# Optimization experiments

Hardware: AMD Instinct MI355X
Metric: run time of the kernel (lower is better)

The kernel has to match this reference:

```python
import jax, jax.numpy as jnp
import numpy as np

N = 100000       # num nodes
E = 1600000      # num edges (avg degree 16)
IN, HID, OUT, C = 128, 64, 64, 16


def setup_inputs() -> dict:
    key = jax.random.key(0)
    ks = jax.random.split(key, 10)
    x = jax.random.normal(ks[0], (N, IN), jnp.float32)
    edge_index = jax.random.randint(ks[1], (2, E), 0, N, dtype=jnp.int32)
    dict_node = jax.random.randint(ks[2], (N,), 0, N, dtype=jnp.int32)
    # learned parameters (Glorot-ish scaling)
    W1 = jax.random.normal(ks[3], (IN, HID), jnp.float32) / np.sqrt(IN)
    b1 = jnp.zeros((HID,), jnp.float32)
    W2 = jax.random.normal(ks[4], (HID, OUT), jnp.float32) / np.sqrt(HID)
    b2 = jnp.zeros((OUT,), jnp.float32)
    Wfc = jax.random.normal(ks[5], (OUT, C), jnp.float32) / np.sqrt(OUT)
    bfc = jnp.zeros((C,), jnp.float32)
    return {"x": x, "edge_index": edge_index, "dict_node": dict_node,
            "W1": W1, "b1": b1, "W2": W2, "b2": b2, "Wfc": Wfc, "bfc": bfc}


def _gcn_conv(h_in, W, b, src, dst, n):
    """GCNConv: D^-1/2 (A+I) D^-1/2 (X W) + b, self-loops handled analytically."""
    h = h_in @ W                                   # [N, F]
    deg = jax.ops.segment_sum(jnp.ones((src.shape[0],), h.dtype), dst,
                              num_segments=n) + 1.0  # +1 self-loop
    dinv = jax.lax.rsqrt(deg)                      # [N]
    norm = dinv[src] * dinv[dst]                   # [E]
    agg = jax.ops.segment_sum(h[src] * norm[:, None], dst, num_segments=n)
    agg = agg + h * (dinv * dinv)[:, None]         # self-loop contribution
    return agg + b


def reference(x, edge_index, dict_node, W1, b1, W2, b2, Wfc, bfc):
    n = x.shape[0]
    src, dst = edge_index[0], edge_index[1]
    h = jax.nn.relu(_gcn_conv(x, W1, b1, src, dst, n))
    # dropout p=0.5 is identity at inference
    h = jax.nn.relu(_gcn_conv(h, W2, b2, src, dst, n))
    # global_mean_pool over dict_node with size = num_nodes
    cnt = jax.ops.segment_sum(jnp.ones((n,), h.dtype), dict_node, num_segments=n)
    summ = jax.ops.segment_sum(h, dict_node, num_segments=n)
    pooled = summ / jnp.maximum(cnt, 1.0)[:, None]
    logits = pooled @ Wfc + bfc
    return jax.nn.log_softmax(logits, axis=1)
```

## Files before the change

kernel.cpp:

```cpp
#include <hip/hip_runtime.h>

#define THREADS 256
#define B1 256

typedef __attribute__((ext_vector_type(8))) short bf16x8;
typedef __attribute__((ext_vector_type(4))) float f32x4;
typedef __attribute__((ext_vector_type(2))) unsigned int u32x2;

__device__ inline ushort f2bf(float v) {
    union { float f; unsigned u; } a; a.f = v;
    unsigned r = a.u + 0x7fff + ((a.u >> 16) & 1);
    return (ushort)(r >> 16);
}
__device__ inline unsigned pack2(float a, float b) {
    return (unsigned)f2bf(a) | ((unsigned)f2bf(b) << 16);
}


__global__ void k_p1(const int* __restrict__ dst, int* __restrict__ pc,
                     int E, int NB, int chunk) {
    __shared__ int hist[512];
    int tid = threadIdx.x, blk = blockIdx.x;
    for (int i = tid; i < NB; i += THREADS) hist[i] = 0;
    __syncthreads();
    int e0 = blk * chunk;
    int e1 = e0 + chunk; if (e1 > E) e1 = E;
    for (int e = e0 + tid; e < e1; e += THREADS)
        atomicAdd(&hist[dst[e] >> 8], 1);
    __syncthreads();
    for (int i = tid; i < NB; i += THREADS) pc[i * B1 + blk] = hist[i];
}

__global__ void k_s1(int* __restrict__ pc, int* __restrict__ bsums, int total) {
    __shared__ int s[1024];
    int t = threadIdx.x;
    int idx = blockIdx.x * 1024 + t;
    int v = (idx < total) ? pc[idx] : 0;
    s[t] = v;
    __syncthreads();
    for (int o = 1; o < 1024; o <<= 1) {
        int x = (t >= (unsigned)o) ? s[t - o] : 0;
        __syncthreads();
        s[t] += x;
        __syncthreads();
    }
    if (idx < total) pc[idx] = s[t] - v;
    if (t == 1023) bsums[blockIdx.x] = s[1023];
}

__global__ void k_s2(int* __restrict__ bsums, int nb) {
    __shared__ int s[128];
    int t = threadIdx.x;
    int v = (t < nb) ? bsums[t] : 0;
    s[t] = v;
    __syncthreads();
    for (int o = 1; o < 128; o <<= 1) {
        int x = (t >= (unsigned)o) ? s[t - o] : 0;
        __syncthreads();
        s[t] += x;
        __syncthreads();
    }
    if (t < nb) bsums[t] = s[t] - v;
}

__global__ void k_p2(const int* __restrict__ src, const int* __restrict__ dst,
                     const int* __restrict__ pc, const int* __restrict__ bsx,
                     unsigned long long* __restrict__ part, int E, int NB, int chunk) {
    __shared__ int cur[512];
    int tid = threadIdx.x, blk = blockIdx.x;
    for (int i = tid; i < NB; i += THREADS) {
        int idx = i * B1 + blk;
        cur[i] = pc[idx] + bsx[idx >> 10];
    }
    __syncthreads();
    int e0 = blk * chunk;
    int e1 = e0 + chunk; if (e1 > E) e1 = E;
    for (int e = e0 + tid; e < e1; e += THREADS) {
        int d = dst[e], sv = src[e];
        int pos = atomicAdd(&cur[d >> 8], 1);
        part[pos] = ((unsigned long long)(unsigned)d << 32) | (unsigned)sv;
    }
}

__global__ void k_p3(const unsigned long long* __restrict__ part,
                     const int* __restrict__ pc, const int* __restrict__ bsx,
                     int* __restrict__ off, float* __restrict__ dinv,
                     int* __restrict__ csr, int E, int NB, int n) {
    __shared__ int hist[256];
    __shared__ int so[256];
    int b = blockIdx.x, t = threadIdx.x;
    int i0 = b * B1, i1 = (b + 1) * B1;
    int base = pc[i0] + bsx[i0 >> 10];
    int end  = (b + 1 < NB) ? (pc[i1] + bsx[i1 >> 10]) : E;
    hist[t] = 0;
    __syncthreads();
    for (int e = base + t; e < end; e += THREADS)
        atomicAdd(&hist[(int)(part[e] >> 32) & 255], 1);
    __syncthreads();
    int h = hist[t];
    so[t] = h;
    __syncthreads();
    for (int o = 1; o < 256; o <<= 1) {
        int x = (t >= (unsigned)o) ? so[t - o] : 0;
        __syncthreads();
        so[t] += x;
        __syncthreads();
    }
    int ex = so[t] - h;
    int node = (b << 8) + t;
    if (node < n) {
        off[node]  = base + ex;
        dinv[node] = rsqrtf((float)h + 1.0f);
        if (node == n - 1) off[n] = E;
    }
    __syncthreads();
    so[t] = base + ex;
    __syncthreads();
    for (int e = base + t; e < end; e += THREADS) {
        unsigned long long p = part[e];
        int pos = atomicAdd(&so[(int)(p >> 32) & 255], 1);
        csr[pos] = (int)(p & 0xffffffffu);
    }
}

template<int KTILES, bool XF32>
__global__ __launch_bounds__(THREADS) void
k_mgemm(const float* __restrict__ Xf, const ushort* __restrict__ Xh,
        const float* __restrict__ W, const float* __restrict__ dinv,
        ushort* __restrict__ C, int n,
        const int* __restrict__ dict, float* __restrict__ cnt,
        int nGemm, int nCnt) {
    int tid = threadIdx.x;
    if ((int)blockIdx.x >= nGemm) {
        int stride = nCnt * THREADS;
        for (int i = ((int)blockIdx.x - nGemm) * THREADS + tid; i < n; i += stride)
            atomicAdd(&cnt[dict[i]], 1.0f);
        return;
    }
    __shared__ ushort wfrag[KTILES * 2048];
    __shared__ float hrow[4][16 * 64];
    const int FIN = KTILES * 32;
    for (int i = tid; i < FIN * 64; i += THREADS) {
        int k = i >> 6, c = i & 63;
        int kk = k >> 5, G = (k >> 3) & 3, e = k & 7;
        int t = c >> 4, c16 = c & 15;
        wfrag[(((kk * 4 + t) * 64) + G * 16 + c16) * 8 + e] = f2bf(W[i]);
    }
    __syncthreads();
    int wslot = tid >> 6, lane = tid & 63;
    int G = lane >> 4, c16 = lane & 15;
    int n0 = blockIdx.x * 64 + wslot * 16;
    int xrow = n0 + c16; if (xrow >= n) xrow = n - 1;
    const bf16x8* wf = (const bf16x8*)wfrag;
    f32x4 acc0 = {0, 0, 0, 0}, acc1 = acc0, acc2 = acc0, acc3 = acc0;
    #pragma unroll
    for (int kk = 0; kk < KTILES; ++kk) {
        bf16x8 a;
        if (XF32) {
            const float* xp = Xf + (size_t)xrow * FIN + kk * 32 + G * 8;
            float4 xa = *(const float4*)xp;
            float4 xb = *(const float4*)(xp + 4);
            a[0] = (short)f2bf(xa.x); a[1] = (short)f2bf(xa.y);
            a[2] = (short)f2bf(xa.z); a[3] = (short)f2bf(xa.w);
            a[4] = (short)f2bf(xb.x); a[5] = (short)f2bf(xb.y);
            a[6] = (short)f2bf(xb.z); a[7] = (short)f2bf(xb.w);
        } else {
            a = *(const bf16x8*)(Xh + (size_t)xrow * FIN + kk * 32 + G * 8);
        }
        bf16x8 b0 = wf[(kk * 4 + 0) * 64 + lane];
        bf16x8 b1 = wf[(kk * 4 + 1) * 64 + lane];
        bf16x8 b2 = wf[(kk * 4 + 2) * 64 + lane];
        bf16x8 b3 = wf[(kk * 4 + 3) * 64 + lane];
        acc0 = __builtin_amdgcn_mfma_f32_16x16x32_bf16(a, b0, acc0, 0, 0, 0);
        acc1 = __builtin_amdgcn_mfma_f32_16x16x32_bf16(a, b1, acc1, 0, 0, 0);
        acc2 = __builtin_amdgcn_mfma_f32_16x16x32_bf16(a, b2, acc2, 0, 0, 0);
        acc3 = __builtin_amdgcn_mfma_f32_16x16x32_bf16(a, b3, acc3, 0, 0, 0);
    }
    int vm = n - n0; if (vm > 16) vm = 16;
    float* hr = &hrow[wslot][0];
    #pragma unroll
    for (int r = 0; r < 4; ++r) {
        int rr = G * 4 + r;
        if (rr < vm) {
            float dn = dinv[n0 + rr];
            hr[rr * 64 + c16]      = acc0[r] * dn;
            hr[rr * 64 + c16 + 16] = acc1[r] * dn;
            hr[rr * 64 + c16 + 32] = acc2[r] * dn;
            hr[rr * 64 + c16 + 48] = acc3[r] * dn;
        }
    }
    asm volatile("" ::: "memory");
    int prow = lane >> 2, pseg = lane & 3;
    if (prow < vm) {
        const float* hp = hr + prow * 64 + pseg * 16;
        float4 f0 = *(const float4*)(hp + 0);
        float4 f1 = *(const float4*)(hp + 4);
        float4 f2 = *(const float4*)(hp + 8);
        float4 f3 = *(const float4*)(hp + 12);
        uint4 o0, o1;
        o0.x = pack2(f0.x, f0.y); o0.y = pack2(f0.z, f0.w);
        o0.z = pack2(f1.x, f1.y); o0.w = pack2(f1.z, f1.w);
        o1.x = pack2(f2.x, f2.y); o1.y = pack2(f2.z, f2.w);
        o1.z = pack2(f3.x, f3.y); o1.w = pack2(f3.z, f3.w);
        ushort* op = C + ((size_t)(n0 + prow) << 6) + pseg * 16;
        *(uint4*)(op)     = o0;
        *(uint4*)(op + 8) = o1;
    }
}

__device__ inline void tr_mfma4(unsigned la, const bf16x8& a,
                                f32x4& o0, f32x4& o1, f32x4& o2, f32x4& o3) {
    u32x2 r0, r1, r2, r3, r4, r5, r6, r7;
    asm volatile(
        "s_waitcnt lgkmcnt(0)\n\t"
        "ds_read_b64_tr_b16 %0, %8 offset:0\n\t"
        "ds_read_b64_tr_b16 %1, %8 offset:512\n\t"
        "ds_read_b64_tr_b16 %2, %8 offset:1024\n\t"
        "ds_read_b64_tr_b16 %3, %8 offset:1536\n\t"
        "ds_read_b64_tr_b16 %4, %8 offset:2048\n\t"
        "ds_read_b64_tr_b16 %5, %8 offset:2560\n\t"
        "ds_read_b64_tr_b16 %6, %8 offset:3072\n\t"
        "ds_read_b64_tr_b16 %7, %8 offset:3584\n\t"
        "s_waitcnt lgkmcnt(0)"
        : "=&v"(r0), "=&v"(r1), "=&v"(r2), "=&v"(r3),
          "=&v"(r4), "=&v"(r5), "=&v"(r6), "=&v"(r7)
        : "v"(la) : "memory");
    __builtin_amdgcn_sched_barrier(0);
    union { u32x2 d[2]; bf16x8 v; } b0, b1, b2, b3;
    b0.d[0] = r0; b0.d[1] = r1; b1.d[0] = r2; b1.d[1] = r3;
    b2.d[0] = r4; b2.d[1] = r5; b3.d[0] = r6; b3.d[1] = r7;
    o0 = __builtin_amdgcn_mfma_f32_16x16x32_bf16(a, b0.v, o0, 0, 0, 0);
    o1 = __builtin_amdgcn_mfma_f32_16x16x32_bf16(a, b1.v, o1, 0, 0, 0);
    o2 = __builtin_amdgcn_mfma_f32_16x16x32_bf16(a, b2.v, o2, 0, 0, 0);
    o3 = __builtin_amdgcn_mfma_f32_16x16x32_bf16(a, b3.v, o3, 0, 0, 0);
}

template<int LAYER>
__global__ __launch_bounds__(THREADS) void
k_agg(const ushort* __restrict__ H, const int* __restrict__ csr,
      const int* __restrict__ off, const float* __restrict__ dinv,
      const float* __restrict__ bias, ushort* __restrict__ outB,
      const float* __restrict__ Wfc, const int* __restrict__ dict,
      float* __restrict__ pool16, int n) {
    __shared__ ushort cbuf[4][2048];
    __shared__ float wt[16 * 65];
    int tid = threadIdx.x;
    if (LAYER == 2) {
        for (int i = tid; i < 64 * 16; i += THREADS) {
            int cc = i >> 4, r = i & 15;
            wt[r * 65 + cc] = Wfc[i];
        }
        __syncthreads();
    }
    int wslot = tid >> 6, lane = tid & 63;
    int gw = blockIdx.x * 4 + wslot;
    int n0 = gw << 4;
    if (n0 >= n) return;
    int G = lane >> 4, c16 = lane & 15;
    int g8 = lane >> 3, q = lane & 7;
    ushort* wbuf = &cbuf[wslot][0];
    unsigned lbase = (unsigned)(size_t)wbuf;
    int vm = n - n0; if (vm > 16) vm = 16;
    int sA = 0, eA = 0;
    if (c16 < vm) { sA = off[n0 + c16]; eA = off[n0 + c16 + 1]; }
    int base0   = __shfl(sA, 0);
    int baseEnd = __shfl(eA, vm - 1);
    unsigned rng = (unsigned)(eA - sA);
    int sb0 = (q >> 1) * 512 + (g8 >> 2) * 256 + (g8 & 3) * 16 + (q & 1) * 8;
    unsigned la = lbase + (unsigned)lane * 8;
    f32x4 acc0 = {0, 0, 0, 0}, acc1 = acc0, acc2 = acc0, acc3 = acc0;

    uint4 cur[4], nxt[4];
    #pragma unroll
    for (int it = 0; it < 4; ++it) {
        uint4 v = {0, 0, 0, 0};
        int k = it * 8 + g8;
        if (base0 + k < baseEnd) {
            int e = csr[base0 + k];
            v = *(const uint4*)(H + ((size_t)e << 6) + q * 8);
        }
        cur[it] = v;
    }
    for (int base = base0; base < baseEnd; base += 32) {
        #pragma unroll
        for (int it = 0; it < 4; ++it) {
            uint4 v = {0, 0, 0, 0};
            int k = base + 32 + it * 8 + g8;
            if (k < baseEnd) {
                int e = csr[k];
                v = *(const uint4*)(H + ((size_t)e << 6) + q * 8);
            }
            nxt[it] = v;
        }
        #pragma unroll
        for (int it = 0; it < 4; ++it)
            *(uint4*)(wbuf + sb0 + it * 64) = cur[it];
        int kb = base - sA;
        bf16x8 a;
        #pragma unroll
        for (int e2 = 0; e2 < 8; ++e2)
            a[e2] = ((unsigned)(G * 8 + e2 + kb) < rng) ? (short)0x3F80 : (short)0;
        tr_mfma4(la, a, acc0, acc1, acc2, acc3);
        #pragma unroll
        for (int it = 0; it < 4; ++it) cur[it] = nxt[it];
    }
    {
        #pragma unroll
        for (int it = 0; it < 4; ++it) {
            uint4 v = {0, 0, 0, 0};
            int k = it * 8 + g8;
            if (it < 2 && k < vm)
                v = *(const uint4*)(H + ((size_t)(n0 + k) << 6) + q * 8);
            *(uint4*)(wbuf + sb0 + it * 64) = v;
        }
        bf16x8 a;
        #pragma unroll
        for (int e2 = 0; e2 < 8; ++e2)
            a[e2] = ((G * 8 + e2) == c16) ? (short)0x3F80 : (short)0;
        tr_mfma4(la, a, acc0, acc1, acc2, acc3);
    }
    float* hrow = (float*)wbuf;
    float bv0 = bias[c16], bv1 = bias[c16 + 16],
          bv2 = bias[c16 + 32], bv3 = bias[c16 + 48];
    #pragma unroll
    for (int r = 0; r < 4; ++r) {
        int rr = G * 4 + r;
        if (rr < vm) {
            float dn = dinv[n0 + rr];
            float v0 = fmaxf(acc0[r] * dn + bv0, 0.f);
            float v1 = fmaxf(acc1[r] * dn + bv1, 0.f);
            float v2 = fmaxf(acc2[r] * dn + bv2, 0.f);
            float v3 = fmaxf(acc3[r] * dn + bv3, 0.f);
            hrow[rr * 64 + c16]      = v0;
            hrow[rr * 64 + c16 + 16] = v1;
            hrow[rr * 64 + c16 + 32] = v2;
            hrow[rr * 64 + c16 + 48] = v3;
        }
    }
    asm volatile("" ::: "memory");
    if (LAYER == 1) {
        int prow = lane >> 2, pseg = lane & 3;
        if (prow < vm) {
            const float* hp = hrow + prow * 64 + pseg * 16;
            float4 f0 = *(const float4*)(hp + 0);
            float4 f1 = *(const float4*)(hp + 4);
            float4 f2 = *(const float4*)(hp + 8);
            float4 f3 = *(const float4*)(hp + 12);
            uint4 o0, o1;
            o0.x = pack2(f0.x, f0.y); o0.y = pack2(f0.z, f0.w);
            o0.z = pack2(f1.x, f1.y); o0.w = pack2(f1.z, f1.w);
            o1.x = pack2(f2.x, f2.y); o1.y = pack2(f2.z, f2.w);
            o1.z = pack2(f3.x, f3.y); o1.w = pack2(f3.z, f3.w);
            ushort* op = outB + ((size_t)(n0 + prow) << 6) + pseg * 16;
            *(uint4*)(op)     = o0;
            *(uint4*)(op + 8) = o1;
        }
    } else {
        int r16 = c16;
        for (int m = 0; m < vm; ++m) {
            const float* hm = hrow + m * 64 + G * 16;
            const float* wr = wt + r16 * 65 + G * 16;
            float p = 0.f;
            #pragma unroll
            for (int i = 0; i < 16; ++i) p = fmaf(hm[i], wr[i], p);
            p += __shfl_xor(p, 16);
            p += __shfl_xor(p, 32);
            if (G == 0)
                atomicAdd(&pool16[(size_t)dict[n0 + m] * 16 + r16], p);
        }
    }
}

__global__ void k_final16(const float* __restrict__ pool16, const float* __restrict__ cnt,
                          const float* __restrict__ bfc, float* __restrict__ out, int n) {
    int tid = threadIdx.x;
    int nl = tid >> 4, lane = tid & 15;
    int node = blockIdx.x * 16 + nl;
    if (node >= n) return;
    float inv = 1.0f / fmaxf(cnt[node], 1.0f);
    float acc = pool16[(size_t)node * 16 + lane] * inv + bfc[lane];
    float m = acc;
    for (int o = 8; o; o >>= 1) m = fmaxf(m, __shfl_xor(m, o, 16));
    float ex = __expf(acc - m);
    float s = ex;
    for (int o = 8; o; o >>= 1) s += __shfl_xor(s, o, 16);
    out[(size_t)node * 16 + lane] = acc - m - __logf(s);
}

extern "C" void kernel_launch(void* const* d_in, const int* in_sizes, int n_in,
                              void* d_out, int out_size, void* d_ws, size_t ws_size,
                              hipStream_t stream) {
    const float* x    = (const float*)d_in[0];
    const int*   ei   = (const int*)d_in[1];
    const int*   dict = (const int*)d_in[2];
    const float* W1   = (const float*)d_in[3];
    const float* b1   = (const float*)d_in[4];
    const float* W2   = (const float*)d_in[5];
    const float* b2   = (const float*)d_in[6];
    const float* Wfc  = (const float*)d_in[7];
    const float* bfc  = (const float*)d_in[8];

    const int N  = in_sizes[2];
    const int E  = in_sizes[1] / 2;
    const int IN = in_sizes[0] / N;
    const int* src = ei;
    const int* dst = ei + E;

    ushort* bufA = (ushort*)d_ws;
    ushort* bufB = bufA + (size_t)N * 64;
    unsigned long long* part = (unsigned long long*)bufB;
    float* dinv    = (float*)(bufB + (size_t)N * 64);
    float* cnt     = dinv + N;
    int*   off     = (int*)(cnt + N);
    int*   pcounts = off + (N + 1);
    const int NB     = (N + 255) >> 8;
    const int pcsize = NB * B1;
    int*   bsums   = pcounts + pcsize;
    int*   csr     = bsums + 128;
    float* pool16  = (float*)(csr + E);

    const int gTile = (N + 63) / 64;
    const int gRows = (N + 15) / 16;
    const int nCnt  = 256;
    const int chunk = (E + B1 - 1) / B1;
    const int nS1   = (pcsize + 1023) >> 10;
    const int gAgg  = ((N + 15) / 16 + 3) / 4;

    hipMemsetAsync(cnt, 0, (size_t)N * sizeof(float), stream);
    hipMemsetAsync(pool16, 0, (size_t)N * 16 * sizeof(float), stream);

    k_p1<<<B1, THREADS, 0, stream>>>(dst, pcounts, E, NB, chunk);
    k_s1<<<nS1, 1024, 0, stream>>>(pcounts, bsums, pcsize);
    k_s2<<<1, 128, 0, stream>>>(bsums, nS1);
    k_p2<<<B1, THREADS, 0, stream>>>(src, dst, pcounts, bsums, part, E, NB, chunk);
    k_p3<<<NB, THREADS, 0, stream>>>(part, pcounts, bsums, off, dinv, csr, E, NB, N);

    k_mgemm<4, true><<<gTile + nCnt, THREADS, 0, stream>>>(
        x, nullptr, W1, dinv, bufA, N, dict, cnt, gTile, nCnt);

    k_agg<1><<<gAgg, THREADS, 0, stream>>>(bufA, csr, off, dinv, b1, bufB,
                                           nullptr, nullptr, nullptr, N);

    k_mgemm<2, false><<<gTile, THREADS, 0, stream>>>(
        nullptr, bufB, W2, dinv, bufA, N, nullptr, nullptr, gTile, 0);
    k_agg<2><<<gAgg, THREADS, 0, stream>>>(bufA, csr, off, dinv, b2, nullptr,
                                           Wfc, dict, pool16, N);

    k_final16<<<gRows, THREADS, 0, stream>>>(pool16, cnt, bfc, (float*)d_out, N);
}
```

Before: 298.8 us.

## Fold memsets into kernels and deepen aggregation gather prefetch to two stages

Drops the two hipMemsetAsync calls. The cnt array is now zeroed inside k_p3, and pool16 is zeroed by extra blocks added to the first GEMM launch, which removes two separate launches. The neighbor-gather loop in k_agg now prefetches two 32-edge batches ahead instead of one, giving more memory-level parallelism to hide gather latency, at the cost of more registers. A launch_bounds occupancy hint of 6 is added to k_agg to keep register use bounded, which risks spills.

```diff
diff --git a/kernel.cpp b/kernel.cpp
--- a/kernel.cpp
+++ b/kernel.cpp
@@ -85,7 +85,8 @@
 __global__ void k_p3(const unsigned long long* __restrict__ part,
                      const int* __restrict__ pc, const int* __restrict__ bsx,
                      int* __restrict__ off, float* __restrict__ dinv,
-                     int* __restrict__ csr, int E, int NB, int n) {
+                     int* __restrict__ csr, float* __restrict__ cnt,
+                     int E, int NB, int n) {
     __shared__ int hist[256];
     __shared__ int so[256];
     int b = blockIdx.x, t = threadIdx.x;
@@ -111,6 +112,7 @@
     if (node < n) {
         off[node]  = base + ex;
         dinv[node] = rsqrtf((float)h + 1.0f);
+        cnt[node]  = 0.0f;
         if (node == n - 1) off[n] = E;
     }
     __syncthreads();
@@ -129,12 +131,22 @@
         const float* __restrict__ W, const float* __restrict__ dinv,
         ushort* __restrict__ C, int n,
         const int* __restrict__ dict, float* __restrict__ cnt,
-        int nGemm, int nCnt) {
+        float* __restrict__ pool16, int nGemm, int nCnt, int nZero) {
     int tid = threadIdx.x;
     if ((int)blockIdx.x >= nGemm) {
-        int stride = nCnt * THREADS;
-        for (int i = ((int)blockIdx.x - nGemm) * THREADS + tid; i < n; i += stride)
-            atomicAdd(&cnt[dict[i]], 1.0f);
+        int rb = (int)blockIdx.x - nGemm;
+        if (rb < nCnt) {
+            int stride = nCnt * THREADS;
+            for (int i = rb * THREADS + tid; i < n; i += stride)
+                atomicAdd(&cnt[dict[i]], 1.0f);
+        } else {
+            int zb = rb - nCnt;
+            uint4* p4 = (uint4*)pool16;
+            int tot = n * 4;
+            int stride = nZero * THREADS;
+            uint4 z = {0, 0, 0, 0};
+            for (int i = zb * THREADS + tid; i < tot; i += stride) p4[i] = z;
+        }
         return;
     }
     __shared__ ushort wfrag[KTILES * 2048];
@@ -236,7 +248,7 @@
 }
 
 template<int LAYER>
-__global__ __launch_bounds__(THREADS) void
+__global__ __launch_bounds__(THREADS, 6) void
 k_agg(const ushort* __restrict__ H, const int* __restrict__ csr,
       const int* __restrict__ off, const float* __restrict__ dinv,
       const float* __restrict__ bias, ushort* __restrict__ outB,
@@ -270,31 +282,41 @@
     unsigned la = lbase + (unsigned)lane * 8;
     f32x4 acc0 = {0, 0, 0, 0}, acc1 = acc0, acc2 = acc0, acc3 = acc0;
 
-    uint4 cur[4], nxt[4];
+    uint4 c0[4], c1[4], c2[4];
     #pragma unroll
     for (int it = 0; it < 4; ++it) {
         uint4 v = {0, 0, 0, 0};
-        int k = it * 8 + g8;
-        if (base0 + k < baseEnd) {
-            int e = csr[base0 + k];
+        int k = base0 + it * 8 + g8;
+        if (k < baseEnd) {
+            int e = csr[k];
             v = *(const uint4*)(H + ((size_t)e << 6) + q * 8);
         }
-        cur[it] = v;
+        c0[it] = v;
+    }
+    #pragma unroll
+    for (int it = 0; it < 4; ++it) {
+        uint4 v = {0, 0, 0, 0};
+        int k = base0 + 32 + it * 8 + g8;
+        if (k < baseEnd) {
+            int e = csr[k];
+            v = *(const uint4*)(H + ((size_t)e << 6) + q * 8);
+        }
+        c1[it] = v;
     }
     for (int base = base0; base < baseEnd; base += 32) {
         #pragma unroll
         for (int it = 0; it < 4; ++it) {
             uint4 v = {0, 0, 0, 0};
-            int k = base + 32 + it * 8 + g8;
+            int k = base + 64 + it * 8 + g8;
             if (k < baseEnd) {
                 int e = csr[k];
                 v = *(const uint4*)(H + ((size_t)e << 6) + q * 8);
             }
-            nxt[it] = v;
+            c2[it] = v;
         }
         #pragma unroll
         for (int it = 0; it < 4; ++it)
-            *(uint4*)(wbuf + sb0 + it * 64) = cur[it];
+            *(uint4*)(wbuf + sb0 + it * 64) = c0[it];
         int kb = base - sA;
         bf16x8 a;
         #pragma unroll
@@ -302,7 +324,7 @@
             a[e2] = ((unsigned)(G * 8 + e2 + kb) < rng) ? (short)0x3F80 : (short)0;
         tr_mfma4(la, a, acc0, acc1, acc2, acc3);
         #pragma unroll
-        for (int it = 0; it < 4; ++it) cur[it] = nxt[it];
+        for (int it = 0; it < 4; ++it) { c0[it] = c1[it]; c1[it] = c2[it]; }
     }
     {
         #pragma unroll
@@ -422,27 +444,26 @@
     const int gTile = (N + 63) / 64;
     const int gRows = (N + 15) / 16;
     const int nCnt  = 256;
+    const int nZero = 256;
     const int chunk = (E + B1 - 1) / B1;
     const int nS1   = (pcsize + 1023) >> 10;
     const int gAgg  = ((N + 15) / 16 + 3) / 4;
-
-    hipMemsetAsync(cnt, 0, (size_t)N * sizeof(float), stream);
-    hipMemsetAsync(pool16, 0, (size_t)N * 16 * sizeof(float), stream);
 
     k_p1<<<B1, THREADS, 0, stream>>>(dst, pcounts, E, NB, chunk);
     k_s1<<<nS1, 1024, 0, stream>>>(pcounts, bsums, pcsize);
     k_s2<<<1, 128, 0, stream>>>(bsums, nS1);
     k_p2<<<B1, THREADS, 0, stream>>>(src, dst, pcounts, bsums, part, E, NB, chunk);
-    k_p3<<<NB, THREADS, 0, stream>>>(part, pcounts, bsums, off, dinv, csr, E, NB, N);
-
-    k_mgemm<4, true><<<gTile + nCnt, THREADS, 0, stream>>>(
-        x, nullptr, W1, dinv, bufA, N, dict, cnt, gTile, nCnt);
+    k_p3<<<NB, THREADS, 0, stream>>>(part, pcounts, bsums, off, dinv, csr, cnt,
+                                     E, NB, N);
+
+    k_mgemm<4, true><<<gTile + nCnt + nZero, THREADS, 0, stream>>>(
+        x, nullptr, W1, dinv, bufA, N, dict, cnt, pool16, gTile, nCnt, nZero);
 
     k_agg<1><<<gAgg, THREADS, 0, stream>>>(bufA, csr, off, dinv, b1, bufB,
                                            nullptr, nullptr, nullptr, N);
 
     k_mgemm<2, false><<<gTile, THREADS, 0, stream>>>(
-        nullptr, bufB, W2, dinv, bufA, N, nullptr, nullptr, gTile, 0);
+        nullptr, bufB, W2, dinv, bufA, N, nullptr, nullptr, nullptr, gTile, 0, 0);
     k_agg<2><<<gAgg, THREADS, 0, stream>>>(bufA, csr, off, dinv, b2, nullptr,
                                            Wfc, dict, pool16, N);
 
```

New measurement: 359.0 us. +20.1%, slower.
